# Kernel tuning notes

Measured on AMD Instinct MI355X. Metric: run time of the kernel, lower is better.

The kernel has to match this reference:

```python
import jax, jax.numpy as jnp
import numpy as np

N_NODES, N_EDGES = 8000, 24000
MUL0_IN, MUL1_IN = 64, 32          # node: 64x0e + 32x1o
MUL0_MSG, MUL1_MSG = 16, 32        # msg:  16x0e + 32x1o
GATE_S, N_GATES = 16, 32           # gate scalars / gates (= mul of 32x1o gated)
RADIAL = 128
EDGE_DIM = 4                       # 1x0e + 1x1o
WNUM = MUL0_IN*MUL0_MSG + MUL0_IN*MUL1_MSG + MUL1_IN*MUL1_MSG + MUL1_IN*MUL0_MSG  # 4608
INV_SQRT3 = 1.0 / np.sqrt(3.0)     # wigner-3j(1,1,0)/(0,1,1)/(1,0,1) magnitude
# e3nn path weights: sqrt(ir_out.dim / sum_paths_into_output(num_elements))
PW_MSG0 = np.sqrt(1.0 / (MUL0_IN + MUL1_IN))                   # tp_msg -> 16x0e
PW_MSG1 = np.sqrt(3.0 / (MUL0_IN + MUL1_IN))                   # tp_msg -> 32x1o
PW_G01 = np.sqrt(1.0 / (MUL0_MSG*MUL0_IN + MUL1_MSG*MUL1_IN))  # FCTP -> 0e outs
PW_G2  = np.sqrt(3.0 / (MUL0_MSG*MUL1_IN + MUL1_MSG*MUL0_IN))  # FCTP -> 1o out
PW_H0 = np.sqrt(1.0 / (GATE_S + MUL1_MSG*MUL1_MSG))            # heavy_tp -> 16x0e
PW_H1 = np.sqrt(3.0 / (GATE_S + GATE_S))                       # heavy_tp -> 32x1o

_trapz = getattr(np, 'trapezoid', np.trapz)
def _cst(f):
    # e3nn normalize2mom constant: 1/sqrt(E_{z~N(0,1)}[f(z)^2])
    xs = np.linspace(-12.0, 12.0, 200001)
    pdf = np.exp(-0.5*xs*xs) / np.sqrt(2.0*np.pi)
    return float(1.0 / np.sqrt(_trapz(f(xs)**2 * pdf, xs)))
CST_SILU = _cst(lambda v: v / (1.0 + np.exp(-v)))
CST_SIG  = _cst(lambda v: 1.0 / (1.0 + np.exp(-v)))
CST_TANH = _cst(np.tanh)


def setup_inputs() -> dict:
    key = jax.random.key(0)
    ks = jax.random.split(key, 19)
    f = lambda k, s: jax.random.normal(k, s, dtype=jnp.float32)
    x = f(ks[0], (N_NODES, MUL0_IN + 3*MUL1_IN))
    edge_attr = f(ks[1], (N_EDGES, EDGE_DIM))
    edge_index = jax.random.randint(ks[2], (2, N_EDGES), 0, N_NODES)
    z = jax.random.randint(ks[3], (N_NODES,), 0, 10)
    canonical = jax.random.randint(ks[4], (N_NODES,), 0, N_NODES)
    W_mlp1 = f(ks[5], (EDGE_DIM, RADIAL))
    W_mlp2 = f(ks[6], (RADIAL, WNUM))
    Wg000 = f(ks[7], (MUL0_MSG, MUL0_IN, GATE_S))
    Wg110 = f(ks[8], (MUL1_MSG, MUL1_IN, GATE_S))
    Wg001 = f(ks[9], (MUL0_MSG, MUL0_IN, N_GATES))
    Wg111 = f(ks[10], (MUL1_MSG, MUL1_IN, N_GATES))
    Wg012 = f(ks[11], (MUL0_MSG, MUL1_IN, MUL1_MSG))
    Wg102 = f(ks[12], (MUL1_MSG, MUL0_IN, MUL1_MSG))
    Wa = f(ks[13], (GATE_S, GATE_S))
    Wb = f(ks[14], (GATE_S, MUL1_MSG))
    Wc = f(ks[15], (MUL1_MSG, GATE_S))
    Wd = f(ks[16], (MUL1_MSG, MUL1_MSG, GATE_S))
    WL0 = f(ks[17], (GATE_S, GATE_S))
    WL1 = f(ks[18], (MUL1_MSG, MUL1_MSG))
    return dict(x=x, edge_attr=edge_attr, W_mlp1=W_mlp1, W_mlp2=W_mlp2,
                Wg000=Wg000, Wg110=Wg110, Wg001=Wg001, Wg111=Wg111,
                Wg012=Wg012, Wg102=Wg102, Wa=Wa, Wb=Wb, Wc=Wc, Wd=Wd,
                WL0=WL0, WL1=WL1, edge_index=edge_index, z=z, canonical=canonical)


def _forward(x, edge_attr, W_mlp1, W_mlp2, Wg000, Wg110, Wg001, Wg111,
             Wg012, Wg102, Wa, Wb, Wc, Wd, WL0, WL1, edge_index, z, canonical):
    N = x.shape[0]
    E = edge_attr.shape[0]
    src, dst = edge_index[0], edge_index[1]
    # ---- radial MLP -> per-edge TP weights (e3nn FullyConnectedNet, normalized silu)
    h = CST_SILU * jax.nn.silu(edge_attr @ (W_mlp1 / np.sqrt(float(EDGE_DIM))))
    w = h @ (W_mlp2 / np.sqrt(float(RADIAL)))                 # (E, 4608)
    s000 = w[:, 0:1024].reshape(E, MUL0_IN, MUL0_MSG)
    s011 = w[:, 1024:3072].reshape(E, MUL0_IN, MUL1_MSG)
    s101 = w[:, 3072:4096].reshape(E, MUL1_IN, MUL1_MSG)
    s110 = w[:, 4096:4608].reshape(E, MUL1_IN, MUL0_MSG)
    # ---- gather source nodes, per-edge equivariant tensor product
    xs0 = x[src, :MUL0_IN]                                    # (E,64)
    xs1 = x[src, MUL0_IN:].reshape(E, MUL1_IN, 3)             # (E,32,3)
    a0 = edge_attr[:, 0]
    a1 = edge_attr[:, 1:4]
    msg0 = PW_MSG0 * (jnp.einsum('e,eu,euw->ew', a0, xs0, s000)
                      + INV_SQRT3 * jnp.einsum('eum,em,euw->ew', xs1, a1, s110))
    msg1 = PW_MSG1 * INV_SQRT3 * (jnp.einsum('eu,em,euw->ewm', xs0, a1, s011)
                                  + jnp.einsum('eum,e,euw->ewm', xs1, a0, s101))
    msg = jnp.concatenate([msg0, msg1.reshape(E, -1)], axis=-1)   # (E,112)
    # ---- scatter_add to destination nodes
    nm = jax.ops.segment_sum(msg, dst, num_segments=N)
    m0 = nm[:, :MUL0_MSG]
    m1 = nm[:, MUL0_MSG:].reshape(N, MUL1_MSG, 3)
    x0 = x[:, :MUL0_IN]
    x1 = x[:, MUL0_IN:].reshape(N, MUL1_IN, 3)
    # ---- FullyConnectedTensorProduct(msg, node) -> scalars | gates | gated
    gs = PW_G01 * (jnp.einsum('nu,nv,uvw->nw', m0, x0, Wg000)
                   + INV_SQRT3 * jnp.einsum('num,nvm,uvw->nw', m1, x1, Wg110))
    gg = PW_G01 * (jnp.einsum('nu,nv,uvw->nw', m0, x0, Wg001)
                   + INV_SQRT3 * jnp.einsum('num,nvm,uvw->nw', m1, x1, Wg111))
    gv = PW_G2 * INV_SQRT3 * (jnp.einsum('nu,nvm,uvw->nwm', m0, x1, Wg012)
                              + jnp.einsum('num,nv,uvw->nwm', m1, x0, Wg102))
    # ---- Gate (normalized sigmoid / tanh)
    xg0 = CST_SIG * jax.nn.sigmoid(gs)                        # (N,16)
    gates = CST_TANH * jnp.tanh(gg)                           # (N,32)
    xg1 = gates[:, :, None] * gv                              # (N,32,3)
    xg = jnp.concatenate([xg0, xg1.reshape(N, -1)], axis=-1)  # (N,112)
    # ---- heavy-atom pooling: scatter_mean of heavy nodes by canonical id
    mask = z > 1
    mf = mask.astype(x.dtype)
    sums = jax.ops.segment_sum(xg * mf[:, None], canonical, num_segments=N)
    cnt = jax.ops.segment_sum(mf, canonical, num_segments=N)
    xh = sums / jnp.maximum(cnt, 1.0)[:, None]
    h0 = xh[:, :GATE_S]
    h1 = xh[:, GATE_S:].reshape(N, MUL1_MSG, 3)
    # ---- heavy self tensor product (internal shared weights)
    t0 = PW_H0 * (jnp.einsum('uv,nu,nv->nu', Wa, h0, h0)
                  + INV_SQRT3 * jnp.einsum('uvw,num,nvm->nw', Wd, h1, h1))
    t1 = PW_H1 * INV_SQRT3 * (jnp.einsum('uv,nu,nvm->nvm', Wb, h0, h1)
                              + jnp.einsum('uv,num,nv->num', Wc, h1, h0))
    th = jnp.concatenate([t0, t1.reshape(N, -1)], axis=-1)
    # ---- broadcast heavy features back to heavy atoms
    y = jnp.where(mask[:, None], th[canonical], xg)
    y0 = y[:, :GATE_S]
    y1 = y[:, GATE_S:].reshape(N, MUL1_MSG, 3)
    # ---- e3nn Linear (per-irrep, 1/sqrt(fan_in))
    out0 = y0 @ (WL0 / np.sqrt(float(GATE_S)))
    out1 = jnp.einsum('num,uw->nwm', y1, WL1) / np.sqrt(float(MUL1_MSG))
    return jnp.concatenate([out0, out1.reshape(N, -1)], axis=-1)  # (N,112)


def reference(x, edge_attr, W_mlp1, W_mlp2, Wg000, Wg110, Wg001, Wg111,
              Wg012, Wg102, Wa, Wb, Wc, Wd, WL0, WL1, edge_index, z, canonical):
    return _forward(x, edge_attr, W_mlp1, W_mlp2, Wg000, Wg110, Wg001, Wg111,
                    Wg012, Wg102, Wa, Wb, Wc, Wd, WL0, WL1, edge_index, z, canonical)
```

## Files before the change

### kernel.cpp

```cpp
#include <hip/hip_runtime.h>
#include <hip/hip_bf16.h>
#include <cmath>


#define N_NODES 8000
#define N_EDGES 24000

#define INV_SQRT3f 0.57735026918962576f
#define PW_MSG0f 0.10206207261596575f
#define PW1f     0.10206207261596575f
#define PW_G01f  0.022097086912079608f
#define PW_G2f   0.034232659844072866f
#define PW_H0f   0.031008683647302115f
#define PW_H1f   0.30618621784789724f
#define RSQRT128f 0.08838834764831845f
#define RSQRT32f  0.17677669529663687f

typedef short short8 __attribute__((ext_vector_type(8)));
typedef short short4v __attribute__((ext_vector_type(4)));
typedef float f32x4 __attribute__((ext_vector_type(4)));

__device__ inline short f32_to_bf16_bits(float v) {
  unsigned int b = __builtin_bit_cast(unsigned int, v);
  b += 0x7fffu + ((b >> 16) & 1u);
  return (short)(b >> 16);
}

__global__ __launch_bounds__(256) void k1_h(const float* __restrict__ ea,
                                            const float* __restrict__ W1,
                                            short* __restrict__ hbf,
                                            float cst_silu) {
  int idx = blockIdx.x * 256 + threadIdx.x;
  int e = idx >> 5, q = idx & 31;
  const float a0 = ea[e*4+0], a1 = ea[e*4+1], a2 = ea[e*4+2], a3 = ea[e*4+3];
  const float4 w0 = *(const float4*)&W1[q*4];
  const float4 w1 = *(const float4*)&W1[128 + q*4];
  const float4 w2 = *(const float4*)&W1[256 + q*4];
  const float4 w3 = *(const float4*)&W1[384 + q*4];
  float s[4] = {0.5f*(a0*w0.x + a1*w1.x + a2*w2.x + a3*w3.x),
                0.5f*(a0*w0.y + a1*w1.y + a2*w2.y + a3*w3.y),
                0.5f*(a0*w0.z + a1*w1.z + a2*w2.z + a3*w3.z),
                0.5f*(a0*w0.w + a1*w1.w + a2*w2.w + a3*w3.w)};
  short4v o;
#pragma unroll
  for (int i = 0; i < 4; ++i) {
    float sg = 1.f / (1.f + expf(-s[i]));
    o[i] = f32_to_bf16_bits(cst_silu * s[i] * sg * RSQRT128f);
  }
  *(short4v*)&hbf[idx*4] = o;
}

__global__ __launch_bounds__(256) void k_prep(const float* __restrict__ W2,
                                              const float* __restrict__ Wg000,
                                              const float* __restrict__ Wg110,
                                              const float* __restrict__ Wg001,
                                              const float* __restrict__ Wg111,
                                              const float* __restrict__ Wg012,
                                              const float* __restrict__ Wg102,
                                              const float* __restrict__ Wd,
                                              const float* __restrict__ WL0,
                                              const float* __restrict__ WL1,
                                              short* __restrict__ w2s,
                                              short* __restrict__ bt,
                                              float* __restrict__ wdt,
                                              float* __restrict__ wl0t,
                                              float* __restrict__ wl1t) {
  const int b = blockIdx.x, tid = threadIdx.x;
  if (b < 576) {
    __shared__ float tile[32][33];
    const int kt = b & 3, ct = b >> 2;
    const int k0 = kt*32, c0 = ct*32;
    const int tx = tid & 31, ty = tid >> 5;
#pragma unroll
    for (int i = 0; i < 4; ++i) {
      int r = ty + i*8;
      tile[r][tx] = W2[(k0+r)*4608 + c0 + tx];
    }
    __syncthreads();
#pragma unroll
    for (int i = 0; i < 4; ++i) {
      int r = ty + i*8;
      const int c = c0 + r, k = k0 + tx;
      const int id = (c < 1024) ? (c >> 4)
                   : (c < 4096) ? ((c + 512) >> 4) : ((c - 3072) >> 4);
      const int nn = c & 15, ks = k >> 5, quad = (k >> 3) & 3, jj = k & 7;
      w2s[id*2048 + ks*512 + (quad*16 + nn)*8 + jj] = f32_to_bf16_bits(tile[tx][r]);
    }
  } else if (b < 1344) {
    int i = (b - 576) * 256 + tid;
    float v;
    if (i < 16384) {
      int col = i >> 6, vv = i & 63, u = col >> 4, w = col & 15;
      v = Wg000[u*1024 + vv*16 + w];
    } else if (i < 49152) {
      int j = i - 16384; int col = j >> 6, vv = j & 63, u = col >> 5, w = col & 31;
      v = Wg001[u*2048 + vv*32 + w];
    } else if (i < 65536) {
      int j = i - 49152; int col = j >> 5, vv = j & 31, u = col >> 4, w = col & 15;
      v = INV_SQRT3f * Wg110[u*512 + vv*16 + w];
    } else if (i < 98304) {
      int j = i - 65536; int col = j >> 5, vv = j & 31, u = col >> 5, w = col & 31;
      v = INV_SQRT3f * Wg111[u*1024 + vv*32 + w];
    } else if (i < 131072) {
      int j = i - 98304; int col = j >> 5, u = j & 31, vv = col >> 5, w = col & 31;
      v = (u < 16) ? Wg012[u*1024 + vv*32 + w] : 0.f;
    } else {
      int j = i - 131072; int col = j >> 6, vv = j & 63, u = col >> 5, w = col & 31;
      v = Wg102[u*2048 + vv*32 + w];
    }
    bt[i] = f32_to_bf16_bits(v);
  } else {
    int i = (b - 1344) * 256 + tid;
    if (i < 16384) {
      int k = i >> 10, uv = i & 1023;
      wdt[i] = Wd[uv*16 + k];
    } else if (i < 16640) {
      int j = i - 16384; int jj = j >> 4, v = j & 15;
      wl0t[j] = WL0[v*16 + jj];
    } else if (i < 17664) {
      int j = i - 16640; int w = j >> 5, u = j & 31;
      wl1t[j] = WL1[u*32 + w];
    }
  }
}

__global__ __launch_bounds__(256, 2) void k2_edge_msg(
    const float* __restrict__ x, const float* __restrict__ ea,
    const short* __restrict__ w2s, const short* __restrict__ hbf,
    const int* __restrict__ ei, float* __restrict__ nm) {
  __shared__ float msg_s[32][116];
  __shared__ float x0pt[64][32];
  __shared__ float z2wt[32][32];
  __shared__ float x1wt[32][32][3];
  __shared__ float a_s[32][4];
  __shared__ int srcs_s[32], dsts_s[32];

  const int tid = threadIdx.x;
  const int e0 = blockIdx.x * 32;

  if (tid < 32) { srcs_s[tid] = ei[e0+tid]; dsts_s[tid] = ei[N_EDGES + e0 + tid]; }
  if (tid < 128) a_s[tid>>2][tid&3] = ea[e0*4 + tid];
  for (int i = tid; i < 32*116; i += 256) (&msg_s[0][0])[i] = 0.f;
  __syncthreads();

  for (int i = tid; i < 2048; i += 256) {
    int e = i >> 6, u = i & 63;
    x0pt[u][e] = PW1f * x[srcs_s[e]*160 + u];
  }
  for (int i = tid; i < 1024; i += 256) {
    int e = i >> 5, u = i & 31;
    const float* xp = &x[srcs_s[e]*160 + 64 + u*3];
    float m0v = xp[0], m1v = xp[1], m2v = xp[2];
    float a0 = a_s[e][0];
    z2wt[u][e] = PW_MSG0f * INV_SQRT3f *
                 (m0v*a_s[e][1] + m1v*a_s[e][2] + m2v*a_s[e][3]);
    x1wt[u][e][0] = PW1f * a0 * m0v;
    x1wt[u][e][1] = PW1f * a0 * m1v;
    x1wt[u][e][2] = PW1f * a0 * m2v;
  }
  __syncthreads();

  const int lane = tid & 63, wv = tid >> 6;
  const int quad = lane >> 4, nn = lane & 15;
  const int eq = quad * 4;

  short8 af[2][4];
#pragma unroll
  for (int t = 0; t < 2; ++t)
#pragma unroll
    for (int ks = 0; ks < 4; ++ks)
      af[t][ks] = *(const short8*)&hbf[(e0 + t*16 + nn)*128 + ks*32 + quad*8];

  float p000[2][4] = {};
  float p0[2][4] = {};
  float p011[2][4] = {};
  float p101[2][4][3] = {};

  short8 Bb[4][4];
  auto loadB = [&](short8* B, int id) {
    const int idc = (id < 287) ? id : 287;
    const short* p = w2s + idc*2048 + lane*8;
    B[0] = *(const short8*)(p);
    B[1] = *(const short8*)(p + 512);
    B[2] = *(const short8*)(p + 1024);
    B[3] = *(const short8*)(p + 1536);
  };
  auto process = [&](const short8* B, int id) {
    f32x4 c0 = {0.f,0.f,0.f,0.f}, c1 = {0.f,0.f,0.f,0.f};
    c0 = __builtin_amdgcn_mfma_f32_16x16x32_bf16(af[0][0], B[0], c0, 0,0,0);
    c1 = __builtin_amdgcn_mfma_f32_16x16x32_bf16(af[1][0], B[0], c1, 0,0,0);
    c0 = __builtin_amdgcn_mfma_f32_16x16x32_bf16(af[0][1], B[1], c0, 0,0,0);
    c1 = __builtin_amdgcn_mfma_f32_16x16x32_bf16(af[1][1], B[1], c1, 0,0,0);
    c0 = __builtin_amdgcn_mfma_f32_16x16x32_bf16(af[0][2], B[2], c0, 0,0,0);
    c1 = __builtin_amdgcn_mfma_f32_16x16x32_bf16(af[1][2], B[2], c1, 0,0,0);
    c0 = __builtin_amdgcn_mfma_f32_16x16x32_bf16(af[0][3], B[3], c0, 0,0,0);
    c1 = __builtin_amdgcn_mfma_f32_16x16x32_bf16(af[1][3], B[3], c1, 0,0,0);
    if (id < 64) {
      const f32x4 w0 = *(const f32x4*)&x0pt[id][eq];
      const f32x4 w1 = *(const f32x4*)&x0pt[id][16 + eq];
#pragma unroll
      for (int r = 0; r < 4; ++r) { p000[0][r] += w0[r]*c0[r]; p000[1][r] += w1[r]*c1[r]; }
    } else if (id < 96) {
      const int u = id - 64;
      const f32x4 w0 = *(const f32x4*)&z2wt[u][eq];
      const f32x4 w1 = *(const f32x4*)&z2wt[u][16 + eq];
#pragma unroll
      for (int r = 0; r < 4; ++r) { p0[0][r] += w0[r]*c0[r]; p0[1][r] += w1[r]*c1[r]; }
    } else if (id < 224) {
      const int u = (id - 96) >> 1;
      const f32x4 w0 = *(const f32x4*)&x0pt[u][eq];
      const f32x4 w1 = *(const f32x4*)&x0pt[u][16 + eq];
#pragma unroll
      for (int r = 0; r < 4; ++r) { p011[0][r] += w0[r]*c0[r]; p011[1][r] += w1[r]*c1[r]; }
    } else {
      const int u = (id - 224) >> 1;
#pragma unroll
      for (int r = 0; r < 4; ++r) {
        const float* xw0 = &x1wt[u][eq + r][0];
        const float* xw1 = &x1wt[u][16 + eq + r][0];
        p101[0][r][0] += xw0[0]*c0[r]; p101[0][r][1] += xw0[1]*c0[r]; p101[0][r][2] += xw0[2]*c0[r];
        p101[1][r][0] += xw1[0]*c1[r]; p101[1][r][1] += xw1[1]*c1[r]; p101[1][r][2] += xw1[2]*c1[r];
      }
    }
  };

  loadB(Bb[0], wv); loadB(Bb[1], wv + 4); loadB(Bb[2], wv + 8);
  int id = wv;
  for (int j = 0; j < 18; ++j) {
    loadB(Bb[3], id + 12); process(Bb[0], id);
    loadB(Bb[0], id + 16); process(Bb[1], id + 4);
    loadB(Bb[1], id + 20); process(Bb[2], id + 8);
    loadB(Bb[2], id + 24); process(Bb[3], id + 12);
    id += 16;
  }

  const int wcol = (wv & 1)*16 + nn;
#pragma unroll
  for (int t = 0; t < 2; ++t)
#pragma unroll
    for (int r = 0; r < 4; ++r) {
      const int e = t*16 + eq + r;
      atomicAdd(&msg_s[e][nn], a_s[e][0]*p000[t][r] + p0[t][r]);
      const float q = p011[t][r];
      atomicAdd(&msg_s[e][16 + wcol*3 + 0], a_s[e][1]*q + p101[t][r][0]);
      atomicAdd(&msg_s[e][16 + wcol*3 + 1], a_s[e][2]*q + p101[t][r][1]);
      atomicAdd(&msg_s[e][16 + wcol*3 + 2], a_s[e][3]*q + p101[t][r][2]);
    }
  __syncthreads();

  for (int i = tid; i < 32*112; i += 256) {
    int le = i / 112, slot = i - le*112;
    atomicAdd(&nm[dsts_s[le]*112 + slot], msg_s[le][slot]);
  }
}

__global__ __launch_bounds__(256, 2) void k3_gate(const float* __restrict__ x,
                                                  const float* __restrict__ nm,
                                                  const short* __restrict__ bt,
                                                  float* __restrict__ xg,
                                                  float cst_sig, float cst_tanh) {
  __shared__ short x0b[16][64];
  __shared__ short x1b[3][16][32];
  __shared__ short m0b[16][32];
  __shared__ float m0t[16][16];
  __shared__ float m1t[32][3][16];
  __shared__ float x1t[32][3][16];
  __shared__ float gs_s[16][20];
  __shared__ float gg_s[16][36];
  __shared__ float gv_s[16][100];
  const int tid = threadIdx.x;
  const int n0 = blockIdx.x * 16;

  for (int i = tid; i < 16*160; i += 256) {
    int n = i / 160, f = i - n*160;
    float v = x[(n0+n)*160 + f];
    if (f < 64) x0b[n][f] = f32_to_bf16_bits(v);
    else {
      int j = f - 64; int vv = j/3, m = j - vv*3;
      x1b[m][n][vv] = f32_to_bf16_bits(v);
      x1t[vv][m][n] = v;
    }
  }
  for (int i = tid; i < 16*112; i += 256) {
    int n = i / 112, f = i - n*112;
    float v = nm[(n0+n)*112 + f];
    if (f < 16) { m0b[n][f] = f32_to_bf16_bits(v); m0t[f][n] = v; }
    else { int j = f - 16; int u = j/3, m = j - u*3; m1t[u][m][n] = v; }
  }
  { int n = tid >> 4, k = tid & 15; m0b[n][16+k] = 0; }
  for (int i = tid; i < 320; i += 256) (&gs_s[0][0])[i] = 0.f;
  for (int i = tid; i < 576; i += 256) (&gg_s[0][0])[i] = 0.f;
  for (int i = tid; i < 1600; i += 256) (&gv_s[0][0])[i] = 0.f;
  __syncthreads();

  const int lane = tid & 63, wv = tid >> 6;
  const int quad = lane >> 4, nn = lane & 15;
  const int eq = quad * 4;
  const int wh = wv & 1;

  const short8 ax0a = *(const short8*)&x0b[nn][quad*8];
  const short8 ax0c = *(const short8*)&x0b[nn][32 + quad*8];
  short8 ax1[3];
#pragma unroll
  for (int m = 0; m < 3; ++m) ax1[m] = *(const short8*)&x1b[m][nn][quad*8];
  const short8 am0 = *(const short8*)&m0b[nn][quad*8];

  const short* b000 = bt;
  const short* b001 = bt + 16384;
  const short* b110 = bt + 49152;
  const short* b111 = bt + 65536;
  const short* b012 = bt + 98304;
  const short* b102 = bt + 131072;

  float gs_p[4] = {}, gg_p[4] = {};
  float gv_p[3][4] = {};

  {
    int u = wv;
    const short* p = b000 + (u*16 + nn)*64 + quad*8;
    short8 ba = *(const short8*)p, bb = *(const short8*)(p + 32);
    for (int i = 0; i < 4; ++i) {
      const int un = (i < 3) ? u + 4 : u;
      const short* np = b000 + (un*16 + nn)*64 + quad*8;
      short8 na = *(const short8*)np, nb2 = *(const short8*)(np + 32);
      f32x4 c = {0.f,0.f,0.f,0.f};
      c = __builtin_amdgcn_mfma_f32_16x16x32_bf16(ax0a, ba, c, 0,0,0);
      c = __builtin_amdgcn_mfma_f32_16x16x32_bf16(ax0c, bb, c, 0,0,0);
      const f32x4 t = *(const f32x4*)&m0t[u][eq];
#pragma unroll
      for (int r = 0; r < 4; ++r) gs_p[r] += t[r]*c[r];
      u = un; ba = na; bb = nb2;
    }
  }
  {
    int u = wv;
    short8 s0 = *(const short8*)(b110 + (u*16 + nn)*32 + quad*8);
    short8 s1 = *(const short8*)(b110 + ((u+4)*16 + nn)*32 + quad*8);
    for (int i = 0; i < 8; i += 2) {
      {
        f32x4 c0 = {0.f,0.f,0.f,0.f}, c1 = {0.f,0.f,0.f,0.f}, c2 = {0.f,0.f,0.f,0.f};
        c0 = __builtin_amdgcn_mfma_f32_16x16x32_bf16(ax1[0], s0, c0, 0,0,0);
        c1 = __builtin_amdgcn_mfma_f32_16x16x32_bf16(ax1[1], s0, c1, 0,0,0);
        c2 = __builtin_amdgcn_mfma_f32_16x16x32_bf16(ax1[2], s0, c2, 0,0,0);
        const f32x4 t0 = *(const f32x4*)&m1t[u][0][eq];
        const f32x4 t1 = *(const f32x4*)&m1t[u][1][eq];
        const f32x4 t2 = *(const f32x4*)&m1t[u][2][eq];
#pragma unroll
        for (int r = 0; r < 4; ++r) gs_p[r] += t0[r]*c0[r] + t1[r]*c1[r] + t2[r]*c2[r];
      }
      { const int up = (i+2 < 8) ? u+8 : u;
        s0 = *(const short8*)(b110 + (up*16 + nn)*32 + quad*8); }
      {
        const int u1 = u + 4;
        f32x4 c0 = {0.f,0.f,0.f,0.f}, c1 = {0.f,0.f,0.f,0.f}, c2 = {0.f,0.f,0.f,0.f};
        c0 = __builtin_amdgcn_mfma_f32_16x16x32_bf16(ax1[0], s1, c0, 0,0,0);
        c1 = __builtin_amdgcn_mfma_f32_16x16x32_bf16(ax1[1], s1, c1, 0,0,0);
        c2 = __builtin_amdgcn_mfma_f32_16x16x32_bf16(ax1[2], s1, c2, 0,0,0);
        const f32x4 t0 = *(const f32x4*)&m1t[u1][0][eq];
        const f32x4 t1 = *(const f32x4*)&m1t[u1][1][eq];
        const f32x4 t2 = *(const f32x4*)&m1t[u1][2][eq];
#pragma unroll
        for (int r = 0; r < 4; ++r) gs_p[r] += t0[r]*c0[r] + t1[r]*c1[r] + t2[r]*c2[r];
      }
      { const int up = (i+3 < 8) ? u+12 : u+4;
        s1 = *(const short8*)(b110 + (up*16 + nn)*32 + quad*8); }
      u += 8;
    }
  }
  {
    int t2 = wv;
    const short* p0p = b001 + ((t2>>1)*32 + wh*16 + nn)*64 + quad*8;
    const short* p1p = b001 + (((t2+4)>>1)*32 + wh*16 + nn)*64 + quad*8;
    short8 a0s = *(const short8*)p0p, b0s = *(const short8*)(p0p + 32);
    short8 a1s = *(const short8*)p1p, b1s = *(const short8*)(p1p + 32);
    for (int i = 0; i < 16; i += 2) {
      {
        f32x4 c = {0.f,0.f,0.f,0.f};
        c = __builtin_amdgcn_mfma_f32_16x16x32_bf16(ax0a, a0s, c, 0,0,0);
        c = __builtin_amdgcn_mfma_f32_16x16x32_bf16(ax0c, b0s, c, 0,0,0);
        const f32x4 t = *(const f32x4*)&m0t[t2>>1][eq];
#pragma unroll
        for (int r = 0; r < 4; ++r) gg_p[r] += t[r]*c[r];
      }
      { const int tp = (i+2 < 16) ? t2+8 : t2;
        const short* np = b001 + ((tp>>1)*32 + wh*16 + nn)*64 + quad*8;
        a0s = *(const short8*)np; b0s = *(const short8*)(np + 32); }
      {
        f32x4 c = {0.f,0.f,0.f,0.f};
        c = __builtin_amdgcn_mfma_f32_16x16x32_bf16(ax0a, a1s, c, 0,0,0);
        c = __builtin_amdgcn_mfma_f32_16x16x32_bf16(ax0c, b1s, c, 0,0,0);
        const f32x4 t = *(const f32x4*)&m0t[(t2+4)>>1][eq];
#pragma unroll
        for (int r = 0; r < 4; ++r) gg_p[r] += t[r]*c[r];
      }
      { const int tp = (i+3 < 16) ? t2+12 : t2+4;
        const short* np = b001 + ((tp>>1)*32 + wh*16 + nn)*64 + quad*8;
        a1s = *(const short8*)np; b1s = *(const short8*)(np + 32); }
      t2 += 8;
    }
  }
  {
    int t2 = wv;
    short8 s0 = *(const short8*)(b111 + ((t2>>1)*32 + wh*16 + nn)*32 + quad*8);
    short8 s1 = *(const short8*)(b111 + (((t2+4)>>1)*32 + wh*16 + nn)*32 + quad*8);
    for (int i = 0; i < 16; i += 2) {
      {
        const int u = t2 >> 1;
        f32x4 c0 = {0.f,0.f,0.f,0.f}, c1 = {0.f,0.f,0.f,0.f}, c2 = {0.f,0.f,0.f,0.f};
        c0 = __builtin_amdgcn_mfma_f32_16x16x32_bf16(ax1[0], s0, c0, 0,0,0);
        c1 = __builtin_amdgcn_mfma_f32_16x16x32_bf16(ax1[1], s0, c1, 0,0,0);
        c2 = __builtin_amdgcn_mfma_f32_16x16x32_bf16(ax1[2], s0, c2, 0,0,0);
        const f32x4 t0 = *(const f32x4*)&m1t[u][0][eq];
        const f32x4 t1 = *(const f32x4*)&m1t[u][1][eq];
        const f32x4 t2v = *(const f32x4*)&m1t[u][2][eq];
#pragma unroll
        for (int r = 0; r < 4; ++r) gg_p[r] += t0[r]*c0[r] + t1[r]*c1[r] + t2v[r]*c2[r];
      }
      { const int tp = (i+2 < 16) ? t2+8 : t2;
        s0 = *(const short8*)(b111 + ((tp>>1)*32 + wh*16 + nn)*32 + quad*8); }
      {
        const int u = (t2+4) >> 1;
        f32x4 c0 = {0.f,0.f,0.f,0.f}, c1 = {0.f,0.f,0.f,0.f}, c2 = {0.f,0.f,0.f,0.f};
        c0 = __builtin_amdgcn_mfma_f32_16x16x32_bf16(ax1[0], s1, c0, 0,0,0);
        c1 = __builtin_amdgcn_mfma_f32_16x16x32_bf16(ax1[1], s1, c1, 0,0,0);
        c2 = __builtin_amdgcn_mfma_f32_16x16x32_bf16(ax1[2], s1, c2, 0,0,0);
        const f32x4 t0 = *(const f32x4*)&m1t[u][0][eq];
        const f32x4 t1 = *(const f32x4*)&m1t[u][1][eq];
        const f32x4 t2v = *(const f32x4*)&m1t[u][2][eq];
#pragma unroll
        for (int r = 0; r < 4; ++r) gg_p[r] += t0[r]*c0[r] + t1[r]*c1[r] + t2v[r]*c2[r];
      }
      { const int tp = (i+3 < 16) ? t2+12 : t2+4;
        s1 = *(const short8*)(b111 + ((tp>>1)*32 + wh*16 + nn)*32 + quad*8); }
      t2 += 8;
    }
  }
  {
    int t2 = wv;
    short8 s0 = *(const short8*)(b012 + ((t2>>1)*32 + wh*16 + nn)*32 + quad*8);
    short8 s1 = *(const short8*)(b012 + (((t2+4)>>1)*32 + wh*16 + nn)*32 + quad*8);
    for (int i = 0; i < 16; i += 2) {
      {
        const int v = t2 >> 1;
        f32x4 c = {0.f,0.f,0.f,0.f};
        c = __builtin_amdgcn_mfma_f32_16x16x32_bf16(am0, s0, c, 0,0,0);
#pragma unroll
        for (int m = 0; m < 3; ++m) {
          const f32x4 t = *(const f32x4*)&x1t[v][m][eq];
#pragma unroll
          for (int r = 0; r < 4; ++r) gv_p[m][r] += t[r]*c[r];
        }
      }
      { const int tp = (i+2 < 16) ? t2+8 : t2;
        s0 = *(const short8*)(b012 + ((tp>>1)*32 + wh*16 + nn)*32 + quad*8); }
      {
        const int v = (t2+4) >> 1;
        f32x4 c = {0.f,0.f,0.f,0.f};
        c = __builtin_amdgcn_mfma_f32_16x16x32_bf16(am0, s1, c, 0,0,0);
#pragma unroll
        for (int m = 0; m < 3; ++m) {
          const f32x4 t = *(const f32x4*)&x1t[v][m][eq];
#pragma unroll
          for (int r = 0; r < 4; ++r) gv_p[m][r] += t[r]*c[r];
        }
      }
      { const int tp = (i+3 < 16) ? t2+12 : t2+4;
        s1 = *(const short8*)(b012 + ((tp>>1)*32 + wh*16 + nn)*32 + quad*8); }
      t2 += 8;
    }
  }
  {
    int t2 = wv;
    const short* p0p = b102 + ((t2>>1)*32 + wh*16 + nn)*64 + quad*8;
    const short* p1p = b102 + (((t2+4)>>1)*32 + wh*16 + nn)*64 + quad*8;
    short8 a0s = *(const short8*)p0p, b0s = *(const short8*)(p0p + 32);
    short8 a1s = *(const short8*)p1p, b1s = *(const short8*)(p1p + 32);
    for (int i = 0; i < 16; i += 2) {
      {
        const int u = t2 >> 1;
        f32x4 c = {0.f,0.f,0.f,0.f};
        c = __builtin_amdgcn_mfma_f32_16x16x32_bf16(ax0a, a0s, c, 0,0,0);
        c = __builtin_amdgcn_mfma_f32_16x16x32_bf16(ax0c, b0s, c, 0,0,0);
#pragma unroll
        for (int m = 0; m < 3; ++m) {
          const f32x4 t = *(const f32x4*)&m1t[u][m][eq];
#pragma unroll
          for (int r = 0; r < 4; ++r) gv_p[m][r] += t[r]*c[r];
        }
      }
      { const int tp = (i+2 < 16) ? t2+8 : t2;
        const short* np = b102 + ((tp>>1)*32 + wh*16 + nn)*64 + quad*8;
        a0s = *(const short8*)np; b0s = *(const short8*)(np + 32); }
      {
        const int u = (t2+4) >> 1;
        f32x4 c = {0.f,0.f,0.f,0.f};
        c = __builtin_amdgcn_mfma_f32_16x16x32_bf16(ax0a, a1s, c, 0,0,0);
        c = __builtin_amdgcn_mfma_f32_16x16x32_bf16(ax0c, b1s, c, 0,0,0);
#pragma unroll
        for (int m = 0; m < 3; ++m) {
          const f32x4 t = *(const f32x4*)&m1t[u][m][eq];
#pragma unroll
          for (int r = 0; r < 4; ++r) gv_p[m][r] += t[r]*c[r];
        }
      }
      { const int tp = (i+3 < 16) ? t2+12 : t2+4;
        const short* np = b102 + ((tp>>1)*32 + wh*16 + nn)*64 + quad*8;
        a1s = *(const short8*)np; b1s = *(const short8*)(np + 32); }
      t2 += 8;
    }
  }

#pragma unroll
  for (int r = 0; r < 4; ++r) {
    atomicAdd(&gs_s[eq + r][nn], gs_p[r]);
    atomicAdd(&gg_s[eq + r][wh*16 + nn], gg_p[r]);
#pragma unroll
    for (int m = 0; m < 3; ++m)
      atomicAdd(&gv_s[eq + r][(wh*16 + nn)*3 + m], gv_p[m][r]);
  }
  __syncthreads();

  for (int i = tid; i < 16*112; i += 256) {
    int n = i / 112, f = i - n*112;
    float o;
    if (f < 16) {
      o = cst_sig / (1.f + expf(-PW_G01f * gs_s[n][f]));
    } else {
      int j = f - 16; int w = j/3;
      float gate = cst_tanh * tanhf(PW_G01f * gg_s[n][w]);
      o = gate * (PW_G2f * INV_SQRT3f) * gv_s[n][j];
    }
    xg[(n0+n)*112 + f] = o;
  }
}

__global__ __launch_bounds__(256) void k4_pool(const float* __restrict__ xg,
                                               const int* __restrict__ z,
                                               const int* __restrict__ canonical,
                                               float* __restrict__ sums,
                                               float* __restrict__ cnt) {
  int idx = blockIdx.x * 256 + threadIdx.x;
  int n = idx / 112, slot = idx - n*112;
  if (z[n] > 1) {
    int c = canonical[n];
    atomicAdd(&sums[c*112 + slot], xg[idx]);
    if (slot == 0) atomicAdd(&cnt[c], 1.f);
  }
}

__global__ __launch_bounds__(256) void k5_thead(const float* __restrict__ sums,
                                                const float* __restrict__ cnt,
                                                const float* __restrict__ Wa,
                                                const float* __restrict__ Wb,
                                                const float* __restrict__ Wc,
                                                const float* __restrict__ wdt,
                                                float* __restrict__ th) {
  __shared__ float xh_s[8][112];
  __shared__ float cm_s[8][1024];
  const int tid = threadIdx.x;
  const int n0 = blockIdx.x * 8;
  for (int i = tid; i < 8*112; i += 256) {
    int n = i / 112, j = i - n*112;
    float cv = fmaxf(cnt[n0+n], 1.f);
    xh_s[n][j] = sums[(n0+n)*112 + j] / cv;
  }
  __syncthreads();
  for (int i = tid; i < 8192; i += 256) {
    int n = i >> 10, uv = i & 1023, u = uv >> 5, v = uv & 31;
    const float* hh = xh_s[n] + 16;
    cm_s[n][uv] = hh[u*3]*hh[v*3] + hh[u*3+1]*hh[v*3+1] + hh[u*3+2]*hh[v*3+2];
  }
  __syncthreads();
  if (tid < 128) {
    int n = tid >> 4, k = tid & 15;
    float sA = 0.f;
    for (int v = 0; v < 16; ++v) sA += Wa[k*16+v]*xh_s[n][v];
    float wd = 0.f;
    const float* cp = cm_s[n];
    const float* wp = wdt + k*1024;
#pragma unroll 4
    for (int uv = 0; uv < 1024; uv += 4) {
      const f32x4 a = *(const f32x4*)&cp[uv];
      const f32x4 bq = *(const f32x4*)&wp[uv];
      wd += a[0]*bq[0] + a[1]*bq[1] + a[2]*bq[2] + a[3]*bq[3];
    }
    th[(n0+n)*112 + k] = PW_H0f*(xh_s[n][k]*sA + INV_SQRT3f*wd);
  }
  {
    int n = tid >> 5, j = tid & 31;
    float wb = 0.f, wc = 0.f;
    for (int u = 0; u < 16; ++u) wb += Wb[u*32+j]*xh_s[n][u];
    for (int v = 0; v < 16; ++v) wc += Wc[j*16+v]*xh_s[n][v];
    float cb = PW_H1f * INV_SQRT3f * (wb + wc);
    const float* hh = xh_s[n] + 16;
    float* o = th + (n0+n)*112 + 16 + j*3;
    o[0] = cb*hh[j*3]; o[1] = cb*hh[j*3+1]; o[2] = cb*hh[j*3+2];
  }
}

__global__ __launch_bounds__(256) void k6_out(const float* __restrict__ xg,
                                              const float* __restrict__ th,
                                              const int* __restrict__ z,
                                              const int* __restrict__ canonical,
                                              const float* __restrict__ wl0t,
                                              const float* __restrict__ wl1t,
                                              float* __restrict__ out) {
  int idx = blockIdx.x * 256 + threadIdx.x;
  int n = idx / 112, j = idx - n*112;
  const float* yr = (z[n] > 1) ? (th + canonical[n]*112) : (xg + n*112);
  float o = 0.f;
  if (j < 16) {
    const float* wp = wl0t + j*16;
#pragma unroll 4
    for (int v = 0; v < 16; ++v) o += yr[v]*wp[v];
    o *= 0.25f;
  } else {
    int jj = j - 16, w = jj / 3, m = jj - w*3;
    const float* wp = wl1t + w*32;
#pragma unroll 4
    for (int u = 0; u < 32; ++u) o += yr[16 + u*3 + m]*wp[u];
    o *= RSQRT32f;
  }
  out[idx] = o;
}

namespace {
struct Csts {
  float silu, sig, tanh_;
  Csts() {
    const int NPT = 200001;
    const double a = -12.0, b = 12.0;
    const double dx = (b - a) / (NPT - 1);
    double s1 = 0.0, s2 = 0.0, s3 = 0.0;
    for (int i = 0; i < NPT; ++i) {
      double xv = a + dx*i;
      double pdf = std::exp(-0.5*xv*xv) / std::sqrt(2.0*M_PI);
      double sg = 1.0 / (1.0 + std::exp(-xv));
      double f1 = xv*sg, f2 = sg, f3 = std::tanh(xv);
      double wg = (i == 0 || i == NPT-1) ? 0.5 : 1.0;
      s1 += wg*f1*f1*pdf; s2 += wg*f2*f2*pdf; s3 += wg*f3*f3*pdf;
    }
    silu  = (float)(1.0/std::sqrt(s1*dx));
    sig   = (float)(1.0/std::sqrt(s2*dx));
    tanh_ = (float)(1.0/std::sqrt(s3*dx));
  }
};
}

extern "C" void kernel_launch(void* const* d_in, const int* in_sizes, int n_in,
                              void* d_out, int out_size, void* d_ws, size_t ws_size,
                              hipStream_t stream) {
  const float* x     = (const float*)d_in[0];
  const float* ea    = (const float*)d_in[1];
  const float* W1    = (const float*)d_in[2];
  const float* W2    = (const float*)d_in[3];
  const float* Wg000 = (const float*)d_in[4];
  const float* Wg110 = (const float*)d_in[5];
  const float* Wg001 = (const float*)d_in[6];
  const float* Wg111 = (const float*)d_in[7];
  const float* Wg012 = (const float*)d_in[8];
  const float* Wg102 = (const float*)d_in[9];
  const float* Wa    = (const float*)d_in[10];
  const float* Wb    = (const float*)d_in[11];
  const float* Wc    = (const float*)d_in[12];
  const float* Wd    = (const float*)d_in[13];
  const float* WL0   = (const float*)d_in[14];
  const float* WL1   = (const float*)d_in[15];
  const int* ei      = (const int*)d_in[16];
  const int* z       = (const int*)d_in[17];
  const int* canonical = (const int*)d_in[18];
  float* out = (float*)d_out;

  float* ws   = (float*)d_ws;
  short* hbf  = (short*)ws;
  short* w2s  = (short*)(ws + 1536000);
  short* bt   = (short*)(ws + 1831000);
  float* nm   = ws + 1930000;
  float* xg   = ws + 2826000;
  float* sums = ws + 3722000;
  float* cnt  = ws + 4618000;
  float* th   = ws + 4626000;
  float* wdt  = ws + 5522000;
  float* wl0t = ws + 5538384;
  float* wl1t = ws + 5538640;

  static const Csts C;

  hipMemsetAsync(nm, 0, 896000*sizeof(float), stream);
  hipMemsetAsync(sums, 0, (896000+8000)*sizeof(float), stream);

  k1_h<<<3000, 256, 0, stream>>>(ea, W1, hbf, C.silu);
  k_prep<<<1413, 256, 0, stream>>>(W2, Wg000, Wg110, Wg001, Wg111, Wg012,
                                   Wg102, Wd, WL0, WL1, w2s, bt, wdt, wl0t, wl1t);
  k2_edge_msg<<<750, 256, 0, stream>>>(x, ea, w2s, hbf, ei, nm);
  k3_gate<<<500, 256, 0, stream>>>(x, nm, bt, xg, C.sig, C.tanh_);
  k4_pool<<<3500, 256, 0, stream>>>(xg, z, canonical, sums, cnt);
  k5_thead<<<1000, 256, 0, stream>>>(sums, cnt, Wa, Wb, Wc, wdt, th);
  k6_out<<<3500, 256, 0, stream>>>(xg, th, z, canonical, wl0t, wl1t, out);
}
```

Measured before the change: 312.0 us.

## Fuse pooling into gate kernel, relayout gate weights, retune edge pipeline

```diff
diff --git a/kernel.cpp b/kernel.cpp
--- a/kernel.cpp
+++ b/kernel.cpp
@@ -90,23 +90,44 @@
     int i = (b - 576) * 256 + tid;
     float v;
     if (i < 16384) {
-      int col = i >> 6, vv = i & 63, u = col >> 4, w = col & 15;
-      v = Wg000[u*1024 + vv*16 + w];
+      int u = i >> 10, r = i & 1023;
+      int ks = r >> 9, lane = (r >> 3) & 63, j = r & 7;
+      int k = ks*32 + (lane >> 4)*8 + j, nn = lane & 15;
+      v = Wg000[u*1024 + k*16 + nn];
     } else if (i < 49152) {
-      int j = i - 16384; int col = j >> 6, vv = j & 63, u = col >> 5, w = col & 31;
-      v = Wg001[u*2048 + vv*32 + w];
+      int o = i - 16384;
+      int tau = o >> 10, r = o & 1023;
+      int u = tau >> 1, wh = tau & 1;
+      int ks = r >> 9, lane = (r >> 3) & 63, j = r & 7;
+      int k = ks*32 + (lane >> 4)*8 + j, nn = lane & 15;
+      v = Wg001[u*2048 + k*32 + wh*16 + nn];
     } else if (i < 65536) {
-      int j = i - 49152; int col = j >> 5, vv = j & 31, u = col >> 4, w = col & 15;
-      v = INV_SQRT3f * Wg110[u*512 + vv*16 + w];
+      int o = i - 49152;
+      int u = o >> 9, r = o & 511;
+      int lane = r >> 3, j = r & 7;
+      int k = (lane >> 4)*8 + j, nn = lane & 15;
+      v = INV_SQRT3f * Wg110[u*512 + k*16 + nn];
     } else if (i < 98304) {
-      int j = i - 65536; int col = j >> 5, vv = j & 31, u = col >> 5, w = col & 31;
-      v = INV_SQRT3f * Wg111[u*1024 + vv*32 + w];
+      int o = i - 65536;
+      int tau = o >> 9, r = o & 511;
+      int u = tau >> 1, wh = tau & 1;
+      int lane = r >> 3, j = r & 7;
+      int k = (lane >> 4)*8 + j, nn = lane & 15;
+      v = INV_SQRT3f * Wg111[u*1024 + k*32 + wh*16 + nn];
     } else if (i < 131072) {
-      int j = i - 98304; int col = j >> 5, u = j & 31, vv = col >> 5, w = col & 31;
-      v = (u < 16) ? Wg012[u*1024 + vv*32 + w] : 0.f;
+      int o = i - 98304;
+      int tau = o >> 9, r = o & 511;
+      int vv = tau >> 1, wh = tau & 1;
+      int lane = r >> 3, j = r & 7;
+      int k = (lane >> 4)*8 + j, nn = lane & 15;
+      v = (k < 16) ? Wg012[k*1024 + vv*32 + wh*16 + nn] : 0.f;
     } else {
-      int j = i - 131072; int col = j >> 6, vv = j & 63, u = col >> 5, w = col & 31;
-      v = Wg102[u*2048 + vv*32 + w];
+      int o = i - 131072;
+      int tau = o >> 10, r = o & 1023;
+      int u = tau >> 1, wh = tau & 1;
+      int ks = r >> 9, lane = (r >> 3) & 63, j = r & 7;
+      int k = ks*32 + (lane >> 4)*8 + j, nn = lane & 15;
+      v = Wg102[u*2048 + k*32 + wh*16 + nn];
     }
     bt[i] = f32_to_bf16_bits(v);
   } else {
@@ -176,7 +197,7 @@
   float p011[2][4] = {};
   float p101[2][4][3] = {};
 
-  short8 Bb[4][4];
+  short8 B0[4], B1[4], B2[4];
   auto loadB = [&](short8* B, int id) {
     const int idc = (id < 287) ? id : 287;
     const short* p = w2s + idc*2048 + lane*8;
@@ -224,14 +245,13 @@
     }
   };
 
-  loadB(Bb[0], wv); loadB(Bb[1], wv + 4); loadB(Bb[2], wv + 8);
+  loadB(B0, wv); loadB(B1, wv + 4);
   int id = wv;
-  for (int j = 0; j < 18; ++j) {
-    loadB(Bb[3], id + 12); process(Bb[0], id);
-    loadB(Bb[0], id + 16); process(Bb[1], id + 4);
-    loadB(Bb[1], id + 20); process(Bb[2], id + 8);
-    loadB(Bb[2], id + 24); process(Bb[3], id + 12);
-    id += 16;
+  for (int j = 0; j < 24; ++j) {
+    loadB(B2, id + 8);  __builtin_amdgcn_sched_barrier(0); process(B0, id);
+    loadB(B0, id + 12); __builtin_amdgcn_sched_barrier(0); process(B1, id + 4);
+    loadB(B1, id + 16); __builtin_amdgcn_sched_barrier(0); process(B2, id + 8);
+    id += 12;
   }
 
   const int wcol = (wv & 1)*16 + nn;
@@ -257,7 +277,11 @@
 __global__ __launch_bounds__(256, 2) void k3_gate(const float* __restrict__ x,
                                                   const float* __restrict__ nm,
                                                   const short* __restrict__ bt,
+                                                  const int* __restrict__ z,
+                                                  const int* __restrict__ canonical,
                                                   float* __restrict__ xg,
+                                                  float* __restrict__ sums,
+                                                  float* __restrict__ cnt,
                                                   float cst_sig, float cst_tanh) {
   __shared__ short x0b[16][64];
   __shared__ short x1b[3][16][32];
@@ -296,7 +320,8 @@
   const int lane = tid & 63, wv = tid >> 6;
   const int quad = lane >> 4, nn = lane & 15;
   const int eq = quad * 4;
-  const int wh = wv & 1;
+  const int wh = wv & 1, uw = wv >> 1;
+  const int l8 = lane * 8;
 
   const short8 ax0a = *(const short8*)&x0b[nn][quad*8];
   const short8 ax0c = *(const short8*)&x0b[nn][32 + quad*8];
@@ -317,196 +342,115 @@
 
   {
     int u = wv;
-    const short* p = b000 + (u*16 + nn)*64 + quad*8;
-    short8 ba = *(const short8*)p, bb = *(const short8*)(p + 32);
+    const short* p = b000 + u*1024 + l8;
+    short8 ba = *(const short8*)p, bb = *(const short8*)(p + 512);
     for (int i = 0; i < 4; ++i) {
       const int un = (i < 3) ? u + 4 : u;
-      const short* np = b000 + (un*16 + nn)*64 + quad*8;
-      short8 na = *(const short8*)np, nb2 = *(const short8*)(np + 32);
+      const short* np = b000 + un*1024 + l8;
+      short8 na = *(const short8*)np, nb = *(const short8*)(np + 512);
+      __builtin_amdgcn_sched_barrier(0);
       f32x4 c = {0.f,0.f,0.f,0.f};
       c = __builtin_amdgcn_mfma_f32_16x16x32_bf16(ax0a, ba, c, 0,0,0);
       c = __builtin_amdgcn_mfma_f32_16x16x32_bf16(ax0c, bb, c, 0,0,0);
       const f32x4 t = *(const f32x4*)&m0t[u][eq];
 #pragma unroll
       for (int r = 0; r < 4; ++r) gs_p[r] += t[r]*c[r];
-      u = un; ba = na; bb = nb2;
+      u = un; ba = na; bb = nb;
     }
   }
   {
     int u = wv;
-    short8 s0 = *(const short8*)(b110 + (u*16 + nn)*32 + quad*8);
-    short8 s1 = *(const short8*)(b110 + ((u+4)*16 + nn)*32 + quad*8);
-    for (int i = 0; i < 8; i += 2) {
-      {
-        f32x4 c0 = {0.f,0.f,0.f,0.f}, c1 = {0.f,0.f,0.f,0.f}, c2 = {0.f,0.f,0.f,0.f};
-        c0 = __builtin_amdgcn_mfma_f32_16x16x32_bf16(ax1[0], s0, c0, 0,0,0);
-        c1 = __builtin_amdgcn_mfma_f32_16x16x32_bf16(ax1[1], s0, c1, 0,0,0);
-        c2 = __builtin_amdgcn_mfma_f32_16x16x32_bf16(ax1[2], s0, c2, 0,0,0);
-        const f32x4 t0 = *(const f32x4*)&m1t[u][0][eq];
-        const f32x4 t1 = *(const f32x4*)&m1t[u][1][eq];
-        const f32x4 t2 = *(const f32x4*)&m1t[u][2][eq];
-#pragma unroll
-        for (int r = 0; r < 4; ++r) gs_p[r] += t0[r]*c0[r] + t1[r]*c1[r] + t2[r]*c2[r];
+    short8 s0 = *(const short8*)(b110 + u*512 + l8);
+    for (int i = 0; i < 8; ++i) {
+      const int un = (i < 7) ? u + 4 : u;
+      short8 ns = *(const short8*)(b110 + un*512 + l8);
+      __builtin_amdgcn_sched_barrier(0);
+      f32x4 c0 = {0.f,0.f,0.f,0.f}, c1 = {0.f,0.f,0.f,0.f}, c2 = {0.f,0.f,0.f,0.f};
+      c0 = __builtin_amdgcn_mfma_f32_16x16x32_bf16(ax1[0], s0, c0, 0,0,0);
+      c1 = __builtin_amdgcn_mfma_f32_16x16x32_bf16(ax1[1], s0, c1, 0,0,0);
+      c2 = __builtin_amdgcn_mfma_f32_16x16x32_bf16(ax1[2], s0, c2, 0,0,0);
+      const f32x4 t0 = *(const f32x4*)&m1t[u][0][eq];
+      const f32x4 t1 = *(const f32x4*)&m1t[u][1][eq];
+      const f32x4 t2 = *(const f32x4*)&m1t[u][2][eq];
+#pragma unroll
+      for (int r = 0; r < 4; ++r) gs_p[r] += t0[r]*c0[r] + t1[r]*c1[r] + t2[r]*c2[r];
+      u = un; s0 = ns;
+    }
+  }
+  {
+    int u = uw;
+    const short* p = b001 + (u*2 + wh)*1024 + l8;
+    short8 ba = *(const short8*)p, bb = *(const short8*)(p + 512);
+    for (int j = 0; j < 8; ++j) {
+      const int un = (j < 7) ? u + 2 : u;
+      const short* np = b001 + (un*2 + wh)*1024 + l8;
+      short8 na = *(const short8*)np, nb = *(const short8*)(np + 512);
+      __builtin_amdgcn_sched_barrier(0);
+      f32x4 c = {0.f,0.f,0.f,0.f};
+      c = __builtin_amdgcn_mfma_f32_16x16x32_bf16(ax0a, ba, c, 0,0,0);
+      c = __builtin_amdgcn_mfma_f32_16x16x32_bf16(ax0c, bb, c, 0,0,0);
+      const f32x4 t = *(const f32x4*)&m0t[u][eq];
+#pragma unroll
+      for (int r = 0; r < 4; ++r) gg_p[r] += t[r]*c[r];
+      u = un; ba = na; bb = nb;
+    }
+  }
+  {
+    int u = uw;
+    short8 s0 = *(const short8*)(b111 + (u*2 + wh)*512 + l8);
+    for (int j = 0; j < 16; ++j) {
+      const int un = (j < 15) ? u + 2 : u;
+      short8 ns = *(const short8*)(b111 + (un*2 + wh)*512 + l8);
+      __builtin_amdgcn_sched_barrier(0);
+      f32x4 c0 = {0.f,0.f,0.f,0.f}, c1 = {0.f,0.f,0.f,0.f}, c2 = {0.f,0.f,0.f,0.f};
+      c0 = __builtin_amdgcn_mfma_f32_16x16x32_bf16(ax1[0], s0, c0, 0,0,0);
+      c1 = __builtin_amdgcn_mfma_f32_16x16x32_bf16(ax1[1], s0, c1, 0,0,0);
+      c2 = __builtin_amdgcn_mfma_f32_16x16x32_bf16(ax1[2], s0, c2, 0,0,0);
+      const f32x4 t0 = *(const f32x4*)&m1t[u][0][eq];
+      const f32x4 t1 = *(const f32x4*)&m1t[u][1][eq];
+      const f32x4 t2 = *(const f32x4*)&m1t[u][2][eq];
+#pragma unroll
+      for (int r = 0; r < 4; ++r) gg_p[r] += t0[r]*c0[r] + t1[r]*c1[r] + t2[r]*c2[r];
+      u = un; s0 = ns;
+    }
+  }
+  {
+    int v = uw;
+    short8 s0 = *(const short8*)(b012 + (v*2 + wh)*512 + l8);
+    for (int j = 0; j < 16; ++j) {
+      const int vn = (j < 15) ? v + 2 : v;
+      short8 ns = *(const short8*)(b012 + (vn*2 + wh)*512 + l8);
+      __builtin_amdgcn_sched_barrier(0);
+      f32x4 c = {0.f,0.f,0.f,0.f};
+      c = __builtin_amdgcn_mfma_f32_16x16x32_bf16(am0, s0, c, 0,0,0);
+#pragma unroll
+      for (int m = 0; m < 3; ++m) {
+        const f32x4 t = *(const f32x4*)&x1t[v][m][eq];
+#pragma unroll
+        for (int r = 0; r < 4; ++r) gv_p[m][r] += t[r]*c[r];
       }
-      { const int up = (i+2 < 8) ? u+8 : u;
-        s0 = *(const short8*)(b110 + (up*16 + nn)*32 + quad*8); }
-      {
-        const int u1 = u + 4;
-        f32x4 c0 = {0.f,0.f,0.f,0.f}, c1 = {0.f,0.f,0.f,0.f}, c2 = {0.f,0.f,0.f,0.f};
-        c0 = __builtin_amdgcn_mfma_f32_16x16x32_bf16(ax1[0], s1, c0, 0,0,0);
-        c1 = __builtin_amdgcn_mfma_f32_16x16x32_bf16(ax1[1], s1, c1, 0,0,0);
-        c2 = __builtin_amdgcn_mfma_f32_16x16x32_bf16(ax1[2], s1, c2, 0,0,0);
-        const f32x4 t0 = *(const f32x4*)&m1t[u1][0][eq];
-        const f32x4 t1 = *(const f32x4*)&m1t[u1][1][eq];
-        const f32x4 t2 = *(const f32x4*)&m1t[u1][2][eq];
-#pragma unroll
-        for (int r = 0; r < 4; ++r) gs_p[r] += t0[r]*c0[r] + t1[r]*c1[r] + t2[r]*c2[r];
+      v = vn; s0 = ns;
+    }
+  }
+  {
+    int u = uw;
+    const short* p = b102 + (u*2 + wh)*1024 + l8;
+    short8 ba = *(const short8*)p, bb = *(const short8*)(p + 512);
+    for (int j = 0; j < 16; ++j) {
+      const int un = (j < 15) ? u + 2 : u;
+      const short* np = b102 + (un*2 + wh)*1024 + l8;
+      short8 na = *(const short8*)np, nb = *(const short8*)(np + 512);
+      __builtin_amdgcn_sched_barrier(0);
+      f32x4 c = {0.f,0.f,0.f,0.f};
+      c = __builtin_amdgcn_mfma_f32_16x16x32_bf16(ax0a, ba, c, 0,0,0);
+      c = __builtin_amdgcn_mfma_f32_16x16x32_bf16(ax0c, bb, c, 0,0,0);
+#pragma unroll
+      for (int m = 0; m < 3; ++m) {
+        const f32x4 t = *(const f32x4*)&m1t[u][m][eq];
+#pragma unroll
+        for (int r = 0; r < 4; ++r) gv_p[m][r] += t[r]*c[r];
       }
-      { const int up = (i+3 < 8) ? u+12 : u+4;
-        s1 = *(const short8*)(b110 + (up*16 + nn)*32 + quad*8); }
-      u += 8;
-    }
-  }
-  {
-    int t2 = wv;
-    const short* p0p = b001 + ((t2>>1)*32 + wh*16 + nn)*64 + quad*8;
-    const short* p1p = b001 + (((t2+4)>>1)*32 + wh*16 + nn)*64 + quad*8;
-    short8 a0s = *(const short8*)p0p, b0s = *(const short8*)(p0p + 32);
-    short8 a1s = *(const short8*)p1p, b1s = *(const short8*)(p1p + 32);
-    for (int i = 0; i < 16; i += 2) {
-      {
-        f32x4 c = {0.f,0.f,0.f,0.f};
-        c = __builtin_amdgcn_mfma_f32_16x16x32_bf16(ax0a, a0s, c, 0,0,0);
-        c = __builtin_amdgcn_mfma_f32_16x16x32_bf16(ax0c, b0s, c, 0,0,0);
-        const f32x4 t = *(const f32x4*)&m0t[t2>>1][eq];
-#pragma unroll
-        for (int r = 0; r < 4; ++r) gg_p[r] += t[r]*c[r];
-      }
-      { const int tp = (i+2 < 16) ? t2+8 : t2;
-        const short* np = b001 + ((tp>>1)*32 + wh*16 + nn)*64 + quad*8;
-        a0s = *(const short8*)np; b0s = *(const short8*)(np + 32); }
-      {
-        f32x4 c = {0.f,0.f,0.f,0.f};
-        c = __builtin_amdgcn_mfma_f32_16x16x32_bf16(ax0a, a1s, c, 0,0,0);
-        c = __builtin_amdgcn_mfma_f32_16x16x32_bf16(ax0c, b1s, c, 0,0,0);
-        const f32x4 t = *(const f32x4*)&m0t[(t2+4)>>1][eq];
-#pragma unroll
-        for (int r = 0; r < 4; ++r) gg_p[r] += t[r]*c[r];
-      }
-      { const int tp = (i+3 < 16) ? t2+12 : t2+4;
-        const short* np = b001 + ((tp>>1)*32 + wh*16 + nn)*64 + quad*8;
-        a1s = *(const short8*)np; b1s = *(const short8*)(np + 32); }
-      t2 += 8;
-    }
-  }
-  {
-    int t2 = wv;
-    short8 s0 = *(const short8*)(b111 + ((t2>>1)*32 + wh*16 + nn)*32 + quad*8);
-    short8 s1 = *(const short8*)(b111 + (((t2+4)>>1)*32 + wh*16 + nn)*32 + quad*8);
-    for (int i = 0; i < 16; i += 2) {
-      {
-        const int u = t2 >> 1;
-        f32x4 c0 = {0.f,0.f,0.f,0.f}, c1 = {0.f,0.f,0.f,0.f}, c2 = {0.f,0.f,0.f,0.f};
-        c0 = __builtin_amdgcn_mfma_f32_16x16x32_bf16(ax1[0], s0, c0, 0,0,0);
-        c1 = __builtin_amdgcn_mfma_f32_16x16x32_bf16(ax1[1], s0, c1, 0,0,0);
-        c2 = __builtin_amdgcn_mfma_f32_16x16x32_bf16(ax1[2], s0, c2, 0,0,0);
-        const f32x4 t0 = *(const f32x4*)&m1t[u][0][eq];
-        const f32x4 t1 = *(const f32x4*)&m1t[u][1][eq];
-        const f32x4 t2v = *(const f32x4*)&m1t[u][2][eq];
-#pragma unroll
-        for (int r = 0; r < 4; ++r) gg_p[r] += t0[r]*c0[r] + t1[r]*c1[r] + t2v[r]*c2[r];
-      }
-      { const int tp = (i+2 < 16) ? t2+8 : t2;
-        s0 = *(const short8*)(b111 + ((tp>>1)*32 + wh*16 + nn)*32 + quad*8); }
-      {
-        const int u = (t2+4) >> 1;
-        f32x4 c0 = {0.f,0.f,0.f,0.f}, c1 = {0.f,0.f,0.f,0.f}, c2 = {0.f,0.f,0.f,0.f};
-        c0 = __builtin_amdgcn_mfma_f32_16x16x32_bf16(ax1[0], s1, c0, 0,0,0);
-        c1 = __builtin_amdgcn_mfma_f32_16x16x32_bf16(ax1[1], s1, c1, 0,0,0);
-        c2 = __builtin_amdgcn_mfma_f32_16x16x32_bf16(ax1[2], s1, c2, 0,0,0);
-        const f32x4 t0 = *(const f32x4*)&m1t[u][0][eq];
-        const f32x4 t1 = *(const f32x4*)&m1t[u][1][eq];
-        const f32x4 t2v = *(const f32x4*)&m1t[u][2][eq];
-#pragma unroll
-        for (int r = 0; r < 4; ++r) gg_p[r] += t0[r]*c0[r] + t1[r]*c1[r] + t2v[r]*c2[r];
-      }
-      { const int tp = (i+3 < 16) ? t2+12 : t2+4;
-        s1 = *(const short8*)(b111 + ((tp>>1)*32 + wh*16 + nn)*32 + quad*8); }
-      t2 += 8;
-    }
-  }
-  {
-    int t2 = wv;
-    short8 s0 = *(const short8*)(b012 + ((t2>>1)*32 + wh*16 + nn)*32 + quad*8);
-    short8 s1 = *(const short8*)(b012 + (((t2+4)>>1)*32 + wh*16 + nn)*32 + quad*8);
-    for (int i = 0; i < 16; i += 2) {
-      {
-        const int v = t2 >> 1;
-        f32x4 c = {0.f,0.f,0.f,0.f};
-        c = __builtin_amdgcn_mfma_f32_16x16x32_bf16(am0, s0, c, 0,0,0);
-#pragma unroll
-        for (int m = 0; m < 3; ++m) {
-          const f32x4 t = *(const f32x4*)&x1t[v][m][eq];
-#pragma unroll
-          for (int r = 0; r < 4; ++r) gv_p[m][r] += t[r]*c[r];
-        }
-      }
-      { const int tp = (i+2 < 16) ? t2+8 : t2;
-        s0 = *(const short8*)(b012 + ((tp>>1)*32 + wh*16 + nn)*32 + quad*8); }
-      {
-        const int v = (t2+4) >> 1;
-        f32x4 c = {0.f,0.f,0.f,0.f};
-        c = __builtin_amdgcn_mfma_f32_16x16x32_bf16(am0, s1, c, 0,0,0);
-#pragma unroll
-        for (int m = 0; m < 3; ++m) {
-          const f32x4 t = *(const f32x4*)&x1t[v][m][eq];
-#pragma unroll
-          for (int r = 0; r < 4; ++r) gv_p[m][r] += t[r]*c[r];
-        }
-      }
-      { const int tp = (i+3 < 16) ? t2+12 : t2+4;
-        s1 = *(const short8*)(b012 + ((tp>>1)*32 + wh*16 + nn)*32 + quad*8); }
-      t2 += 8;
-    }
-  }
-  {
-    int t2 = wv;
-    const short* p0p = b102 + ((t2>>1)*32 + wh*16 + nn)*64 + quad*8;
-    const short* p1p = b102 + (((t2+4)>>1)*32 + wh*16 + nn)*64 + quad*8;
-    short8 a0s = *(const short8*)p0p, b0s = *(const short8*)(p0p + 32);
-    short8 a1s = *(const short8*)p1p, b1s = *(const short8*)(p1p + 32);
-    for (int i = 0; i < 16; i += 2) {
-      {
-        const int u = t2 >> 1;
-        f32x4 c = {0.f,0.f,0.f,0.f};
-        c = __builtin_amdgcn_mfma_f32_16x16x32_bf16(ax0a, a0s, c, 0,0,0);
-        c = __builtin_amdgcn_mfma_f32_16x16x32_bf16(ax0c, b0s, c, 0,0,0);
-#pragma unroll
-        for (int m = 0; m < 3; ++m) {
-          const f32x4 t = *(const f32x4*)&m1t[u][m][eq];
-#pragma unroll
-          for (int r = 0; r < 4; ++r) gv_p[m][r] += t[r]*c[r];
-        }
-      }
-      { const int tp = (i+2 < 16) ? t2+8 : t2;
-        const short* np = b102 + ((tp>>1)*32 + wh*16 + nn)*64 + quad*8;
-        a0s = *(const short8*)np; b0s = *(const short8*)(np + 32); }
-      {
-        const int u = (t2+4) >> 1;
-        f32x4 c = {0.f,0.f,0.f,0.f};
-        c = __builtin_amdgcn_mfma_f32_16x16x32_bf16(ax0a, a1s, c, 0,0,0);
-        c = __builtin_amdgcn_mfma_f32_16x16x32_bf16(ax0c, b1s, c, 0,0,0);
-#pragma unroll
-        for (int m = 0; m < 3; ++m) {
-          const f32x4 t = *(const f32x4*)&m1t[u][m][eq];
-#pragma unroll
-          for (int r = 0; r < 4; ++r) gv_p[m][r] += t[r]*c[r];
-        }
-      }
-      { const int tp = (i+3 < 16) ? t2+12 : t2+4;
-        const short* np = b102 + ((tp>>1)*32 + wh*16 + nn)*64 + quad*8;
-        a1s = *(const short8*)np; b1s = *(const short8*)(np + 32); }
-      t2 += 8;
+      u = un; ba = na; bb = nb;
     }
   }
 
@@ -530,21 +474,13 @@
       float gate = cst_tanh * tanhf(PW_G01f * gg_s[n][w]);
       o = gate * (PW_G2f * INV_SQRT3f) * gv_s[n][j];
     }
-    xg[(n0+n)*112 + f] = o;
-  }
-}
-
-__global__ __launch_bounds__(256) void k4_pool(const float* __restrict__ xg,
-                                               const int* __restrict__ z,
-                                               const int* __restrict__ canonical,
-                                               float* __restrict__ sums,
-                                               float* __restrict__ cnt) {
-  int idx = blockIdx.x * 256 + threadIdx.x;
-  int n = idx / 112, slot = idx - n*112;
-  if (z[n] > 1) {
-    int c = canonical[n];
-    atomicAdd(&sums[c*112 + slot], xg[idx]);
-    if (slot == 0) atomicAdd(&cnt[c], 1.f);
+    const int gn = n0 + n;
+    xg[gn*112 + f] = o;
+    if (z[gn] > 1) {
+      const int c = canonical[gn];
+      atomicAdd(&sums[c*112 + f], o);
+      if (f == 0) atomicAdd(&cnt[c], 1.f);
+    }
   }
 }
 
@@ -557,6 +493,7 @@
                                                 float* __restrict__ th) {
   __shared__ float xh_s[8][112];
   __shared__ float cm_s[8][1024];
+  __shared__ float red[256];
   const int tid = threadIdx.x;
   const int n0 = blockIdx.x * 8;
   for (int i = tid; i < 8*112; i += 256) {
@@ -571,19 +508,26 @@
     cm_s[n][uv] = hh[u*3]*hh[v*3] + hh[u*3+1]*hh[v*3+1] + hh[u*3+2]*hh[v*3+2];
   }
   __syncthreads();
+  {
+    const int hs = tid >> 7, p = tid & 127;
+    const int n = p >> 4, k = p & 15;
+    float wd = 0.f;
+    const float* cp = cm_s[n] + hs*512;
+    const float* wp = wdt + k*1024 + hs*512;
+#pragma unroll 4
+    for (int uv = 0; uv < 512; uv += 4) {
+      const f32x4 a = *(const f32x4*)&cp[uv];
+      const f32x4 bq = *(const f32x4*)&wp[uv];
+      wd += a[0]*bq[0] + a[1]*bq[1] + a[2]*bq[2] + a[3]*bq[3];
+    }
+    red[tid] = wd;
+  }
+  __syncthreads();
   if (tid < 128) {
     int n = tid >> 4, k = tid & 15;
     float sA = 0.f;
     for (int v = 0; v < 16; ++v) sA += Wa[k*16+v]*xh_s[n][v];
-    float wd = 0.f;
-    const float* cp = cm_s[n];
-    const float* wp = wdt + k*1024;
-#pragma unroll 4
-    for (int uv = 0; uv < 1024; uv += 4) {
-      const f32x4 a = *(const f32x4*)&cp[uv];
-      const f32x4 bq = *(const f32x4*)&wp[uv];
-      wd += a[0]*bq[0] + a[1]*bq[1] + a[2]*bq[2] + a[3]*bq[3];
-    }
+    float wd = red[tid] + red[tid + 128];
     th[(n0+n)*112 + k] = PW_H0f*(xh_s[n][k]*sA + INV_SQRT3f*wd);
   }
   {
@@ -693,8 +637,8 @@
   k_prep<<<1413, 256, 0, stream>>>(W2, Wg000, Wg110, Wg001, Wg111, Wg012,
                                    Wg102, Wd, WL0, WL1, w2s, bt, wdt, wl0t, wl1t);
   k2_edge_msg<<<750, 256, 0, stream>>>(x, ea, w2s, hbf, ei, nm);
-  k3_gate<<<500, 256, 0, stream>>>(x, nm, bt, xg, C.sig, C.tanh_);
-  k4_pool<<<3500, 256, 0, stream>>>(xg, z, canonical, sums, cnt);
+  k3_gate<<<500, 256, 0, stream>>>(x, nm, bt, z, canonical, xg, sums, cnt,
+                                   C.sig, C.tanh_);
   k5_thead<<<1000, 256, 0, stream>>>(sums, cnt, Wa, Wb, Wc, wdt, th);
   k6_out<<<3500, 256, 0, stream>>>(xg, th, z, canonical, wl0t, wl1t, out);
 }
```

Result: faster. 288.4 us (-7.6%).
